# Performance work log

Hardware: AMD Instinct MI355X
Metric: run time of the kernel (lower is better)

Reference implementation:

```python
import jax, jax.numpy as jnp
import numpy as np

NEG_SLOPE = 0.01  # torch nn.LeakyReLU default


def setup_inputs() -> dict:
    key = jax.random.key(0)
    k1, k2 = jax.random.split(key)
    B, L, N = 32, 512, 1024
    X = jax.random.normal(k1, (B, L, N), dtype=jnp.float32)
    W = jax.random.normal(k2, (1, 2 * L), dtype=jnp.float32) * (1.0 / np.sqrt(2 * L))
    return {"X": X, "W": W}


def reference(X, W):
    # X: [B, L, N]; W: [1, 2L] weight of Linear(2L, 1, bias=False)
    L = X.shape[1]
    N = X.shape[2]
    w1 = W[0, :L]   # applied to X[:, :, i]
    w2 = W[0, L:]   # applied to X[:, :, j]
    s1 = jnp.einsum('bln,l->bn', X, w1)  # [B, N]
    s2 = jnp.einsum('bln,l->bn', X, w2)  # [B, N]
    # e[b,i,j] = leaky_relu(s1[b,i] + s2[b,j]) for i != j, 0 on the diagonal
    e = jax.nn.leaky_relu(s1[:, :, None] + s2[:, None, :], NEG_SLOPE)  # [B, N, N]
    diag = jnp.eye(N, dtype=bool)
    e = jnp.where(diag[None, :, :], 0.0, e)
    # softmax over dim=1 (over i), matching torch.softmax(e, dim=1)
    alpha = jax.nn.softmax(e, axis=1)  # [B, N, N]
    # h = bmm(alpha, X^T)^T: h[b,l,i] = sum_j alpha[b,i,j] * X[b,l,j]
    h = jnp.einsum('bij,blj->bli', alpha, X)  # [B, L, N]
    return jax.nn.sigmoid(h)
```

## Files before the change

### kernel.cpp

```cpp
#include <hip/hip_runtime.h>
#include <hip/hip_bf16.h>

#define BATCH 32
#define LSEQ  512
#define NDIM  1024
#define NSPLIT 32

typedef __attribute__((ext_vector_type(8))) short bf16x8;
typedef __attribute__((ext_vector_type(4))) float f32x4;

__device__ __forceinline__ unsigned short f2bf(float x) {
    __hip_bfloat16 h = __float2bfloat16(x);
    return __builtin_bit_cast(unsigned short, h);
}

__global__ __launch_bounds__(256) void prep_kernel(
    const float* __restrict__ X, const float* __restrict__ W,
    unsigned short* __restrict__ Xb, float* __restrict__ P1, float* __restrict__ P2)
{
    __shared__ float sw[2 * LSEQ];
    int tid = threadIdx.x;
    for (int i = tid; i < 2 * LSEQ; i += 256) sw[i] = W[i];
    __syncthreads();

    int b  = blockIdx.y;
    int sp = blockIdx.x;
    int l0 = sp * (LSEQ / NSPLIT);
    size_t base = ((size_t)b * LSEQ + l0) * NDIM + tid * 4;
    const float* xp = X + base;
    unsigned short* xbp = Xb + base;

    float a0=0,a1=0,a2=0,a3=0, c0=0,c1=0,c2=0,c3=0;
    #pragma unroll
    for (int l = 0; l < LSEQ / NSPLIT; ++l) {
        float4 x = *(const float4*)(xp + (size_t)l * NDIM);
        float w1 = sw[l0 + l], w2 = sw[LSEQ + l0 + l];
        a0 = fmaf(x.x, w1, a0); a1 = fmaf(x.y, w1, a1);
        a2 = fmaf(x.z, w1, a2); a3 = fmaf(x.w, w1, a3);
        c0 = fmaf(x.x, w2, c0); c1 = fmaf(x.y, w2, c1);
        c2 = fmaf(x.z, w2, c2); c3 = fmaf(x.w, w2, c3);
        ushort4 u; u.x = f2bf(x.x); u.y = f2bf(x.y); u.z = f2bf(x.z); u.w = f2bf(x.w);
        *(ushort4*)(xbp + (size_t)l * NDIM) = u;
    }
    size_t po = ((size_t)sp * BATCH + b) * NDIM + tid * 4;
    *(float4*)(P1 + po) = make_float4(a0, a1, a2, a3);
    *(float4*)(P2 + po) = make_float4(c0, c1, c2, c3);
}

__global__ __launch_bounds__(256) void stats_kernel(
    const float* __restrict__ P1, const float* __restrict__ P2,
    float* __restrict__ s1, float* __restrict__ s2, float* __restrict__ lrd)
{
    __shared__ float s1s[NDIM];
    __shared__ float s2s[128];
    int t = threadIdx.x;
    int b = blockIdx.x >> 3, sl = blockIdx.x & 7;
    int j0 = sl * 128;

    #pragma unroll
    for (int q = 0; q < 4; ++q) {
        int n = q * 256 + t;
        float a = 0.f;
        #pragma unroll
        for (int sp = 0; sp < NSPLIT; ++sp)
            a += P1[((size_t)sp * BATCH + b) * NDIM + n];
        s1s[n] = a;
        if (sl == 0) s1[b * NDIM + n] = a;
    }
    if (t < 128) {
        int j = j0 + t;
        float c = 0.f;
        #pragma unroll
        for (int sp = 0; sp < NSPLIT; ++sp)
            c += P2[((size_t)sp * BATCH + b) * NDIM + j];
        s2s[t] = c;
        s2[b * NDIM + j] = c;
    }
    __syncthreads();

    int jl = t >> 1, half = t & 1;
    int jg = j0 + jl;
    float s2j = s2s[jl];
    float sum = 0.f;
    int i0 = half * 512;
    for (int i = i0; i < i0 + 512; ++i) {
        float v = s1s[i] + s2j;
        v = fmaxf(v, 0.01f * v);
        if (i == jg) v = 0.f;
        sum += __expf(v);
    }
    sum += __shfl_xor(sum, 1);
    if (half == 0) lrd[b * NDIM + jg] = -__logf(sum);
}

#define WAITVM0() asm volatile("s_waitcnt vmcnt(0)" ::: "memory")
#define LGKM0()   asm volatile("s_waitcnt lgkmcnt(0)" ::: "memory")
#define BARF()    do { asm volatile("" ::: "memory");                          \
                       __builtin_amdgcn_s_barrier();                           \
                       asm volatile("" ::: "memory"); } while (0)

#define STAGE(DB) {                                                            \
    _Pragma("unroll")                                                          \
    for (int j = 0; j < 4; ++j) {                                              \
        __builtin_amdgcn_global_load_lds(                                      \
            (const __attribute__((address_space(1))) void*)srcp[j],            \
            (__attribute__((address_space(3))) void*)(LdsC + (DB) * 32768 +    \
                tid * 16 + j * 8192), 16, 0, 0);                               \
        srcp[j] += 128;                                  \
    } }

#define BGEN(T2, DB) {                                                         \
    const float* s2p = s2s + (T2) * 64 + jb * 8;                               \
    const float* ldp = lrds + (T2) * 64 + jb * 8;                              \
    float4 sa = *(const float4*)(s2p);                                         \
    float4 sb = *(const float4*)(s2p + 4);                                     \
    float4 la = *(const float4*)(ldp);                                         \
    float4 lb = *(const float4*)(ldp + 4);                                     \
    float sv[8] = {sa.x,sa.y,sa.z,sa.w,sb.x,sb.y,sb.z,sb.w};                   \
    float lv[8] = {la.x,la.y,la.z,la.w,lb.x,lb.y,lb.z,lb.w};                   \
    int jg0 = (T2) * 64 + jb * 8;                                              \
    _Pragma("unroll")                                                          \
    for (int q = 0; q < 4; ++q) {                                              \
        int rloc = wid * 32 + q * 8 + il;                                      \
        int ig = n0 + rloc;                                                    \
        bf16x8 w;                                                              \
        _Pragma("unroll")                                                      \
        for (int h = 0; h < 8; ++h) {                                          \
            float v = s1q[q] + sv[h];                                          \
            v = fmaxf(v, 0.01f * v);                           \
            if (jg0 + h == ig) v = 0.f;                  \
            w[h] = (short)f2bf(__expf(v + lv[h]));                             \
        }                                                                      \
        *(bf16x8*)(LdsC + 65536 + (DB) * 32768 + rloc * 128 +                  \
                   ((jb * 16) ^ (il << 4))) = w;                               \
    } }

#define COMPUTE_KS(DB, KOF) {                                                  \
    bf16x8 av[8], bv[4];                                                       \
    _Pragma("unroll")                                                          \
    for (int mi = 0; mi < 8; ++mi)                                             \
        av[mi] = *(const bf16x8*)(LdsC + (DB) * 32768 + arow + mi * 2048 +     \
                                  (KOF));                                      \
    _Pragma("unroll")                                                          \
    for (int ni = 0; ni < 4; ++ni)                                             \
        bv[ni] = *(const bf16x8*)(LdsC + 65536 + (DB) * 32768 + brow +         \
                                  ni * 2048 + (KOF));                          \
    __builtin_amdgcn_s_setprio(1);                                             \
    _Pragma("unroll")                                                          \
    for (int ni = 0; ni < 4; ++ni)                                             \
        _Pragma("unroll")                                                      \
        for (int mi = 0; mi < 8; ++mi)                                         \
            acc[mi][ni] = __builtin_amdgcn_mfma_f32_16x16x32_bf16(             \
                av[mi], bv[ni], acc[mi][ni], 0, 0, 0);                         \
    __builtin_amdgcn_s_setprio(0);                                             \
}

__global__ __launch_bounds__(512, 2) void gemm_kernel(
    const unsigned short* __restrict__ Xb, const float* __restrict__ s1,
    const float* __restrict__ s2, const float* __restrict__ lrd,
    float* __restrict__ out)
{
    __shared__ __align__(16) char LdsC[139264];
    float* s2s  = (float*)(LdsC + 131072);
    float* lrds = (float*)(LdsC + 135168);

    const int tid = threadIdx.x, lane = tid & 63, wid = tid >> 6;
    const int wm = wid >> 2, wn = wid & 3;

    int flat  = blockIdx.x;
    int xcd   = flat & 7;
    int p     = flat >> 3;
    int b     = (p >> 3) * 8 + xcd;
    int inner = p & 7;
    int mt = inner & 1, nt = inner >> 1;
    int l0 = mt * 256, n0 = nt * 256;

    const char* XgB = (const char*)(Xb + ((size_t)b * LSEQ + l0) * NDIM);

    const char* srcp[4];
    #pragma unroll
    for (int j = 0; j < 4; ++j) {
        int c = tid + j * 512;
        int r = c >> 3, slot = c & 7;
        srcp[j] = XgB + (size_t)r * 2048 + ((slot * 16) ^ ((r & 7) << 4));
    }

    const int rsel = lane & 15, kq = lane >> 4;
    const int swz  = (rsel & 7) << 4;
    const int kof0 = (kq * 16) ^ swz;
    const int kof1 = (64 + kq * 16) ^ swz;
    const int arow = (wm * 128 + rsel) * 128;
    const int brow = (wn * 64 + rsel) * 128;

    const int jb = lane & 7, il = lane >> 3;

    {
        const float* s2g = s2 + (size_t)b * NDIM;
        const float* ldg = lrd + (size_t)b * NDIM;
        if (tid < 256) *(float4*)(s2s + tid * 4) = *(const float4*)(s2g + tid * 4);
        else *(float4*)(lrds + (tid - 256) * 4) = *(const float4*)(ldg + (tid - 256) * 4);
    }
    STAGE(0);
    __syncthreads();

    float s1q[4];
    #pragma unroll
    for (int q = 0; q < 4; ++q)
        s1q[q] = s1[(size_t)b * NDIM + n0 + wid * 32 + q * 8 + il];

    f32x4 acc[8][4] = {};

    BGEN(0, 0);
    LGKM0(); BARF();

    for (int t = 0; t < 15; ++t) {
        int db = t & 1, dn = db ^ 1;
        STAGE(dn);
        COMPUTE_KS(db, kof0);
        BGEN(t + 1, dn);
        COMPUTE_KS(db, kof1);
        LGKM0(); WAITVM0(); BARF();
    }
    COMPUTE_KS(1, kof0);
    COMPUTE_KS(1, kof1);

    float* outb = out + ((size_t)b * LSEQ + l0) * NDIM + n0;
    const int rq = lane >> 4, cl = lane & 15;
    #pragma unroll
    for (int mi = 0; mi < 8; ++mi)
        #pragma unroll
        for (int ni = 0; ni < 4; ++ni) {
            int col = wn * 64 + ni * 16 + cl;
            #pragma unroll
            for (int r2 = 0; r2 < 4; ++r2) {
                int row = wm * 128 + mi * 16 + rq * 4 + r2;
                float v = acc[mi][ni][r2];
                outb[(size_t)row * NDIM + col] = 1.0f / (1.0f + __expf(-v));
            }
        }
}

#undef WAITVM0
#undef LGKM0
#undef BARF
#undef STAGE
#undef BGEN
#undef COMPUTE_KS

extern "C" void kernel_launch(void* const* d_in, const int* in_sizes, int n_in,
                              void* d_out, int out_size, void* d_ws, size_t ws_size,
                              hipStream_t stream) {
    (void)in_sizes; (void)n_in; (void)out_size; (void)ws_size;
    const float* X = (const float*)d_in[0];
    const float* W = (const float*)d_in[1];
    float* out = (float*)d_out;

    float* s1 = (float*)d_ws;
    float* s2 = s1 + BATCH * NDIM;
    float* lrd = s2 + BATCH * NDIM;
    float* P1 = lrd + BATCH * NDIM;
    float* P2 = P1 + (size_t)NSPLIT * BATCH * NDIM;
    unsigned short* Xb = (unsigned short*)(P2 + (size_t)NSPLIT * BATCH * NDIM);

    prep_kernel<<<dim3(NSPLIT, BATCH), 256, 0, stream>>>(X, W, Xb, P1, P2);
    stats_kernel<<<256, 256, 0, stream>>>(P1, P2, s1, s2, lrd);
    gemm_kernel<<<256, 512, 0, stream>>>(Xb, s1, s2, lrd, out);
}
```

Baseline: 189.1 us.

## Shrink GEMM tile to 256x128 with 4 waves and K-step 32

Reworks the attention GEMM to use 256-thread blocks over 256x128 output tiles with a K step of 32 instead of 64, doubling the grid to 512 blocks and cutting LDS use from ~136KB to ~56KB per block. A new swizzled LDS layout packs two rows per 128-byte line, and a single compute per iteration replaces the two half-K computes. The prep kernel also halves NSPLIT and drops its loop unroll. The aim is more resident blocks per CU and better occupancy and load balance. The cost is twice as many barrier iterations, the A operand being reloaded for each of the two N tiles, and a larger share of exp work in the B generation per MFMA.

```diff
diff --git a/kernel.cpp b/kernel.cpp
--- a/kernel.cpp
+++ b/kernel.cpp
@@ -4,7 +4,7 @@
 #define BATCH 32
 #define LSEQ  512
 #define NDIM  1024
-#define NSPLIT 32
+#define NSPLIT 16
 
 typedef __attribute__((ext_vector_type(8))) short bf16x8;
 typedef __attribute__((ext_vector_type(4))) float f32x4;
@@ -31,7 +31,6 @@
     unsigned short* xbp = Xb + base;
 
     float a0=0,a1=0,a2=0,a3=0, c0=0,c1=0,c2=0,c3=0;
-    #pragma unroll
     for (int l = 0; l < LSEQ / NSPLIT; ++l) {
         float4 x = *(const float4*)(xp + (size_t)l * NDIM);
         float w1 = sw[l0 + l], w2 = sw[LSEQ + l0 + l];
@@ -99,52 +98,51 @@
                        __builtin_amdgcn_s_barrier();                           \
                        asm volatile("" ::: "memory"); } while (0)
 
-#define STAGE(DB) {                                                            \
+#define STAGE(DN) {                                                            \
     _Pragma("unroll")                                                          \
     for (int j = 0; j < 4; ++j) {                                              \
         __builtin_amdgcn_global_load_lds(                                      \
             (const __attribute__((address_space(1))) void*)srcp[j],            \
-            (__attribute__((address_space(3))) void*)(LdsC + (DB) * 32768 +    \
-                tid * 16 + j * 8192), 16, 0, 0);                               \
-        srcp[j] += 128;                                  \
+            (__attribute__((address_space(3))) void*)(LdsC + (DN) * 16384 +    \
+                tid * 16 + j * 4096), 16, 0, 0);                               \
+        srcp[j] += 64;                               \
     } }
 
-#define BGEN(T2, DB) {                                                         \
-    const float* s2p = s2s + (T2) * 64 + jb * 8;                               \
-    const float* ldp = lrds + (T2) * 64 + jb * 8;                              \
+#define BGEN(TT, DN) {                                                         \
+    int k0f = (TT) * 32;                                                       \
+    const float* s2p = s2s + k0f + jb8;                                        \
+    const float* ldp = lrds + k0f + jb8;                                       \
     float4 sa = *(const float4*)(s2p);                                         \
     float4 sb = *(const float4*)(s2p + 4);                                     \
     float4 la = *(const float4*)(ldp);                                         \
     float4 lb = *(const float4*)(ldp + 4);                                     \
     float sv[8] = {sa.x,sa.y,sa.z,sa.w,sb.x,sb.y,sb.z,sb.w};                   \
     float lv[8] = {la.x,la.y,la.z,la.w,lb.x,lb.y,lb.z,lb.w};                   \
-    int jg0 = (T2) * 64 + jb * 8;                                              \
-    _Pragma("unroll")                                                          \
-    for (int q = 0; q < 4; ++q) {                                              \
-        int rloc = wid * 32 + q * 8 + il;                                      \
-        int ig = n0 + rloc;                                                    \
+    _Pragma("unroll")                                                          \
+    for (int q2 = 0; q2 < 2; ++q2) {                                           \
+        int ig = n0 + rloc0 + q2 * 64;                                         \
+        float s1i = s1v[q2];                                                   \
         bf16x8 w;                                                              \
         _Pragma("unroll")                                                      \
         for (int h = 0; h < 8; ++h) {                                          \
-            float v = s1q[q] + sv[h];                                          \
+            float v = s1i + sv[h];                                             \
             v = fmaxf(v, 0.01f * v);                           \
-            if (jg0 + h == ig) v = 0.f;                  \
+            if (k0f + jb8 + h == ig) v = 0.f;            \
             w[h] = (short)f2bf(__expf(v + lv[h]));                             \
         }                                                                      \
-        *(bf16x8*)(LdsC + 65536 + (DB) * 32768 + rloc * 128 +                  \
-                   ((jb * 16) ^ (il << 4))) = w;                               \
+        *(bf16x8*)(LdsC + 32768 + (DN) * 8192 + srbase + q2 * 4096 + bgin) = w;\
     } }
 
-#define COMPUTE_KS(DB, KOF) {                                                  \
+#define COMPUTE(DD) {                                                          \
+    const char* La = LdsC + (DD) * 16384;                                      \
+    const char* Lb = LdsC + 32768 + (DD) * 8192;                               \
     bf16x8 av[8], bv[4];                                                       \
     _Pragma("unroll")                                                          \
     for (int mi = 0; mi < 8; ++mi)                                             \
-        av[mi] = *(const bf16x8*)(LdsC + (DB) * 32768 + arow + mi * 2048 +     \
-                                  (KOF));                                      \
+        av[mi] = *(const bf16x8*)(La + abase0 + mi * 1024);                    \
     _Pragma("unroll")                                                          \
     for (int ni = 0; ni < 4; ++ni)                                             \
-        bv[ni] = *(const bf16x8*)(LdsC + 65536 + (DB) * 32768 + brow +         \
-                                  ni * 2048 + (KOF));                          \
+        bv[ni] = *(const bf16x8*)(Lb + bbase0 + ni * 1024);                    \
     __builtin_amdgcn_s_setprio(1);                                             \
     _Pragma("unroll")                                                          \
     for (int ni = 0; ni < 4; ++ni)                                             \
@@ -155,74 +153,75 @@
     __builtin_amdgcn_s_setprio(0);                                             \
 }
 
-__global__ __launch_bounds__(512, 2) void gemm_kernel(
+__global__ __launch_bounds__(256, 2) void gemm_kernel(
     const unsigned short* __restrict__ Xb, const float* __restrict__ s1,
     const float* __restrict__ s2, const float* __restrict__ lrd,
     float* __restrict__ out)
 {
-    __shared__ __align__(16) char LdsC[139264];
-    float* s2s  = (float*)(LdsC + 131072);
-    float* lrds = (float*)(LdsC + 135168);
+    __shared__ __align__(16) char LdsC[57344];
+    float* s2s  = (float*)(LdsC + 49152);
+    float* lrds = (float*)(LdsC + 53248);
 
     const int tid = threadIdx.x, lane = tid & 63, wid = tid >> 6;
-    const int wm = wid >> 2, wn = wid & 3;
+    const int wm = wid >> 1, wn = wid & 1;
 
     int flat  = blockIdx.x;
     int xcd   = flat & 7;
     int p     = flat >> 3;
-    int b     = (p >> 3) * 8 + xcd;
-    int inner = p & 7;
+    int b     = (p >> 4) * 8 + xcd;
+    int inner = p & 15;
     int mt = inner & 1, nt = inner >> 1;
-    int l0 = mt * 256, n0 = nt * 256;
+    int l0 = mt * 256, n0 = nt * 128;
 
     const char* XgB = (const char*)(Xb + ((size_t)b * LSEQ + l0) * NDIM);
 
     const char* srcp[4];
     #pragma unroll
     for (int j = 0; j < 4; ++j) {
-        int c = tid + j * 512;
-        int r = c >> 3, slot = c & 7;
-        srcp[j] = XgB + (size_t)r * 2048 + ((slot * 16) ^ ((r & 7) << 4));
+        int c = tid + j * 256;
+        int sr = c >> 3, slot = c & 7;
+        int li = (slot * 16) ^ ((sr & 7) << 4);
+        int r = sr * 2 + (li >> 6);
+        srcp[j] = XgB + (size_t)r * 2048 + (li & 63);
     }
 
     const int rsel = lane & 15, kq = lane >> 4;
-    const int swz  = (rsel & 7) << 4;
-    const int kof0 = (kq * 16) ^ swz;
-    const int kof1 = (64 + kq * 16) ^ swz;
-    const int arow = (wm * 128 + rsel) * 128;
-    const int brow = (wn * 64 + rsel) * 128;
-
-    const int jb = lane & 7, il = lane >> 3;
+    const int finner = (((rsel & 1) * 64) + kq * 16) ^ (((rsel >> 1) & 7) << 4);
+    const int abase0 = (wm * 64 + (rsel >> 1)) * 128 + finner;
+    const int bbase0 = (wn * 32 + (rsel >> 1)) * 128 + finner;
+
+    const int rloc0 = wid * 16 + (lane & 15);
+    const int jb8   = (lane >> 4) * 8;
+    const int srbase = (rloc0 >> 1) * 128;
+    const int bgin  = (((rloc0 & 1) * 64) + (lane >> 4) * 16)
+                      ^ (((rloc0 >> 1) & 7) << 4);
 
     {
         const float* s2g = s2 + (size_t)b * NDIM;
         const float* ldg = lrd + (size_t)b * NDIM;
-        if (tid < 256) *(float4*)(s2s + tid * 4) = *(const float4*)(s2g + tid * 4);
-        else *(float4*)(lrds + (tid - 256) * 4) = *(const float4*)(ldg + (tid - 256) * 4);
+        *(float4*)(s2s + tid * 4)  = *(const float4*)(s2g + tid * 4);
+        *(float4*)(lrds + tid * 4) = *(const float4*)(ldg + tid * 4);
     }
     STAGE(0);
     __syncthreads();
 
-    float s1q[4];
-    #pragma unroll
-    for (int q = 0; q < 4; ++q)
-        s1q[q] = s1[(size_t)b * NDIM + n0 + wid * 32 + q * 8 + il];
+    float s1v[2];
+    s1v[0] = s1[(size_t)b * NDIM + n0 + rloc0];
+    s1v[1] = s1[(size_t)b * NDIM + n0 + rloc0 + 64];
 
     f32x4 acc[8][4] = {};
 
     BGEN(0, 0);
     LGKM0(); BARF();
 
-    for (int t = 0; t < 15; ++t) {
-        int db = t & 1, dn = db ^ 1;
+    for (int t = 0; t < 31; ++t) {
+        int d = t & 1, dn = d ^ 1;
         STAGE(dn);
-        COMPUTE_KS(db, kof0);
         BGEN(t + 1, dn);
-        COMPUTE_KS(db, kof1);
+        COMPUTE(d);
         LGKM0(); WAITVM0(); BARF();
     }
-    COMPUTE_KS(1, kof0);
-    COMPUTE_KS(1, kof1);
+    COMPUTE(1);
 
     float* outb = out + ((size_t)b * LSEQ + l0) * NDIM + n0;
     const int rq = lane >> 4, cl = lane & 15;
@@ -245,7 +244,7 @@
 #undef BARF
 #undef STAGE
 #undef BGEN
-#undef COMPUTE_KS
+#undef COMPUTE
 
 extern "C" void kernel_launch(void* const* d_in, const int* in_sizes, int n_in,
                               void* d_out, int out_size, void* d_ws, size_t ws_size,
@@ -264,5 +263,5 @@
 
     prep_kernel<<<dim3(NSPLIT, BATCH), 256, 0, stream>>>(X, W, Xb, P1, P2);
     stats_kernel<<<256, 256, 0, stream>>>(P1, P2, s1, s2, lrd);
-    gemm_kernel<<<256, 512, 0, stream>>>(Xb, s1, s2, lrd, out);
-}
+    gemm_kernel<<<512, 256, 0, stream>>>(Xb, s1, s2, lrd, out);
+}
```

New measurement: 173.5 us. 8.2% less time.
